# Kernel optimization log

Hardware: AMD Instinct MI355X
Metric: run time of the kernel (lower is better)

Reference implementation:

```python
import jax, jax.numpy as jnp
import numpy as np

B, N, IN_DIM, OUT_DIM = 16, 2048, 512, 512

def _xavier(key, shape):
    bound = float(np.sqrt(6.0 / (shape[0] + shape[1])))
    return jax.random.uniform(key, shape, jnp.float32, -bound, bound)

def setup_inputs() -> dict:
    key = jax.random.key(0)
    kx, kk, kq, kv = jax.random.split(key, 4)
    return {
        "x": jax.random.normal(kx, (B, N, IN_DIM), jnp.float32),
        "W_key": _xavier(kk, (IN_DIM, OUT_DIM)),
        "W_query": _xavier(kq, (IN_DIM, OUT_DIM)),
        "W_value": _xavier(kv, (IN_DIM, OUT_DIM)),
    }

def reference(x, W_key, W_query, W_value):
    # projections: [B, N, out_dim]
    k = jnp.matmul(x, W_key)
    q = jnp.matmul(x, W_query)
    v = jnp.matmul(x, W_value)
    scale = jnp.sqrt(jnp.asarray(IN_DIM, jnp.float32))
    scores = jnp.einsum("bnd,bmd->bnm", q, k) / scale  # [B, N, N]
    weights = jax.nn.softmax(scores, axis=2)
    attn = jnp.einsum("bnm,bmd->bnd", weights, v)  # [B, N, out_dim]
    return jnp.mean(attn, axis=1)  # [B, out_dim]
```

## Files before the change

### kernel.cpp

```cpp
#include <hip/hip_runtime.h>
#include <hip/hip_bf16.h>
#include <hip/hip_fp16.h>
#include <stdint.h>

#define NB 16
#define NN 2048
#define ND 512
#define SSCALE 0.044194173824159216f

typedef unsigned short u16;
typedef unsigned int u32;
typedef float f32x4 __attribute__((ext_vector_type(4)));
typedef __bf16 bf16x8 __attribute__((ext_vector_type(8)));
typedef unsigned short u16x8 __attribute__((ext_vector_type(8)));

__device__ __forceinline__ float bf2f(u16 h) {
  union { u32 u; float f; } v; v.u = ((u32)h) << 16; return v.f;
}
__device__ __forceinline__ u16 f2bf(float f) {
  union { float f; u32 u; } v; v.f = f;
  u32 r = v.u + 0x7fffu + ((v.u >> 16) & 1u);
  return (u16)(r >> 16);
}
__device__ __forceinline__ u16 f2h(float f) {
  __half h = __float2half(f);
  union { __half h; u16 u; } v; v.h = h; return v.u;
}
__device__ __forceinline__ float h2f(u16 u) {
  union { u16 u; __half h; } v; v.u = u; return __half2float(v.h);
}

__device__ __forceinline__ void async16(const void* g, void* l) {
  __builtin_amdgcn_global_load_lds(
      (const __attribute__((address_space(1))) u32*)g,
      (__attribute__((address_space(3))) u32*)l,
      16, 0, 0);
}

template <int MODE, bool AF32>
__global__ __launch_bounds__(256, 2) void gemm_bt(
    const void* __restrict__ Av, const u16* __restrict__ B, u16* __restrict__ C,
    float* __restrict__ Lrow, int lda, int ldb, int ldc, int K,
    long long sA, long long sB, long long sC, float cscale) {
  const int tid  = threadIdx.x;
  const int w    = tid >> 6;
  const int lane = tid & 63;
  const int wm   = w >> 1, wn = w & 1;
  const int lrow = lane & 15, quad = lane >> 4;
  const long long z = blockIdx.z;

  const float* Abf = (const float*)Av + z * sA + (size_t)blockIdx.y * 128 * lda;
  const u16*   Abh = (const u16*)Av   + z * sA + (size_t)blockIdx.y * 128 * lda;
  const u16*   Bb  = B + z * sB + (size_t)blockIdx.x * 128 * ldb;

  __shared__ __align__(16) u16 lds_a[128 * 32];
  __shared__ __align__(16) u16 lds_b[128 * 32];

  f32x4 acc[4][4];
#pragma unroll
  for (int i = 0; i < 4; i++)
#pragma unroll
    for (int j = 0; j < 4; j++) acc[i][j] = (f32x4){0.f, 0.f, 0.f, 0.f};

  for (int k0 = 0; k0 < K; k0 += 32) {
    if (k0) __syncthreads();
    if (AF32) {
      u16x8 va[2];
#pragma unroll
      for (int t = 0; t < 2; t++) {
        int ch  = t * 256 + tid;
        int row = ch >> 2;
        int cc  = (ch & 3) * 8;
        const float4* p = (const float4*)(Abf + (size_t)row * lda + k0 + cc);
        float4 f0 = p[0], f1 = p[1];
        u16x8 r;
        r[0] = f2bf(f0.x); r[1] = f2bf(f0.y); r[2] = f2bf(f0.z); r[3] = f2bf(f0.w);
        r[4] = f2bf(f1.x); r[5] = f2bf(f1.y); r[6] = f2bf(f1.z); r[7] = f2bf(f1.w);
        va[t] = r;
        async16(Bb + (size_t)row * ldb + k0 + cc, &lds_b[ch * 8]);
      }
#pragma unroll
      for (int t = 0; t < 2; t++) *(u16x8*)&lds_a[(t * 256 + tid) * 8] = va[t];
    } else {
#pragma unroll
      for (int t = 0; t < 2; t++) {
        int ch  = t * 256 + tid;
        int row = ch >> 2;
        int cc  = (ch & 3) * 8;
        async16(Abh + (size_t)row * lda + k0 + cc, &lds_a[ch * 8]);
        async16(Bb  + (size_t)row * ldb + k0 + cc, &lds_b[ch * 8]);
      }
    }
    __syncthreads();

    bf16x8 af[4], bfr[4];
#pragma unroll
    for (int i = 0; i < 4; i++) {
      af[i]  = *(const bf16x8*)&lds_a[(wm * 64 + i * 16 + lrow) * 32 + quad * 8];
      bfr[i] = *(const bf16x8*)&lds_b[(wn * 64 + i * 16 + lrow) * 32 + quad * 8];
    }
#pragma unroll
    for (int i = 0; i < 4; i++)
#pragma unroll
      for (int j = 0; j < 4; j++)
        acc[i][j] =
            __builtin_amdgcn_mfma_f32_16x16x32_bf16(af[i], bfr[j], acc[i][j], 0, 0, 0);
  }

  u16* Cb = C + z * sC + (size_t)blockIdx.y * 128 * ldc + (size_t)blockIdx.x * 128;
  if (MODE == 0) {
#pragma unroll
    for (int i = 0; i < 4; i++)
#pragma unroll
      for (int j = 0; j < 4; j++)
#pragma unroll
        for (int r = 0; r < 4; r++) {
          int row = wm * 64 + i * 16 + quad * 4 + r;
          int col = wn * 64 + j * 16 + lrow;
          Cb[(size_t)row * ldc + col] = f2bf(acc[i][j][r] * cscale);
        }
  } else {
    float* Lb = Lrow + z * NN + (size_t)blockIdx.y * 128;
#pragma unroll
    for (int i = 0; i < 4; i++)
#pragma unroll
      for (int r = 0; r < 4; r++) {
        int row = wm * 64 + i * 16 + quad * 4 + r;
        float rs = 0.f;
#pragma unroll
        for (int j = 0; j < 4; j++) {
          int col = wn * 64 + j * 16 + lrow;
          float e = __expf(fminf(acc[i][j][r] * cscale, 10.f));
          Cb[(size_t)row * ldc + col] = f2h(e);
          rs += e;
        }
        rs += __shfl_xor(rs, 1); rs += __shfl_xor(rs, 2);
        rs += __shfl_xor(rs, 4); rs += __shfl_xor(rs, 8);
        if (lrow == 0) atomicAdd(&Lb[row], rs);
      }
  }
}

__device__ __forceinline__ void stage_half(const u16* __restrict__ g, int ld,
                                           int row0, int k0,
                                           u16* __restrict__ l, int tid) {
  int r  = tid >> 3;
  int Lc = (tid & 7) ^ (r & 7);
  async16(g + (size_t)(row0 + r) * ld + k0 + Lc * 8, l + tid * 8);
  async16(g + (size_t)(row0 + 64 + r) * ld + k0 + Lc * 8, l + 4096 + tid * 8);
}

__device__ __forceinline__ bf16x8 ldf(const u16* __restrict__ h, int rbase,
                                      int lrow, int quad, int ks) {
  int rr = rbase + lrow;
  int pc = (ks * 4 + quad) ^ (lrow & 7);
  return *(const bf16x8*)&h[rr * 64 + pc * 8];
}

#define BAR() __builtin_amdgcn_s_barrier()
#define WAIT_LGKM()                                          \
  do {                                                       \
    asm volatile("s_waitcnt lgkmcnt(0)" ::: "memory");       \
    __builtin_amdgcn_sched_barrier(0);                       \
  } while (0)

#define READ_A(p, mh)                                                        \
  _Pragma("unroll") for (int i2 = 0; i2 < 4; ++i2)                           \
  _Pragma("unroll") for (int ks = 0; ks < 2; ++ks)                           \
      af[i2][ks] = ldf(sm + (p) * 32768 + wm * 8192, ((mh)*4 + i2) * 16,     \
                       lrow, quad, ks);

#define READ_B(p, nh)                                                        \
  _Pragma("unroll") for (int j2 = 0; j2 < 2; ++j2)                           \
  _Pragma("unroll") for (int ks = 0; ks < 2; ++ks)                           \
      bq[(nh)*2 + j2][ks] =                                                  \
          ldf(sm + (p) * 32768 + 16384 + (wn >> 1) * 8192,                   \
              (wn & 1) * 64 + ((nh)*2 + j2) * 16, lrow, quad, ks);

#define MFMA_Q(mh, nh)                                                       \
  __builtin_amdgcn_s_setprio(1);                                             \
  _Pragma("unroll") for (int i2 = 0; i2 < 4; ++i2)                           \
  _Pragma("unroll") for (int j2 = 0; j2 < 2; ++j2)                           \
  _Pragma("unroll") for (int ks = 0; ks < 2; ++ks)                           \
      acc[(mh)*4 + i2][(nh)*2 + j2] = __builtin_amdgcn_mfma_f32_16x16x32_bf16( \
          af[i2][ks], bq[(nh)*2 + j2][ks], acc[(mh)*4 + i2][(nh)*2 + j2],    \
          0, 0, 0);                                                          \
  __builtin_amdgcn_s_setprio(0);

#define STAGE_A(p, h, kt) \
  stage_half(Ab, lda, (h)*128, (kt)*64, sm + (p)*32768 + (h)*8192, tid)
#define STAGE_B(p, h, kt) \
  stage_half(Bb, ldb, (h)*128, (kt)*64, sm + (p)*32768 + 16384 + (h)*8192, tid)

template <int MODE>
__global__ __launch_bounds__(512, 2) void gemm256(
    const u16* __restrict__ A, const u16* __restrict__ B, u16* __restrict__ C,
    float* __restrict__ Lrow, int lda, int ldb, int ldc, int K,
    long long sA, long long sB, long long sC, float cscale) {
  const int tid  = threadIdx.x;
  const int wid  = tid >> 6, lane = tid & 63;
  const int wm   = wid >> 2, wn = wid & 3;
  const int lrow = lane & 15, quad = lane >> 4;

  const int bxx = blockIdx.x;
  const int byy = blockIdx.y;
  const long long z = blockIdx.z;

  const u16* Ab = A + z * sA + (size_t)byy * 256 * lda;
  const u16* Bb = B + z * sB + (size_t)bxx * 256 * ldb;

  __shared__ __align__(16) u16 sm[65536];

  f32x4 acc[8][4];
#pragma unroll
  for (int i = 0; i < 8; i++)
#pragma unroll
    for (int j = 0; j < 4; j++) acc[i][j] = (f32x4){0.f, 0.f, 0.f, 0.f};

  bf16x8 af[4][2];
  bf16x8 bq[4][2];

  const int NITER = K >> 7;

  STAGE_A(0, 0, 0); STAGE_A(0, 1, 0);
  STAGE_B(0, 0, 0); STAGE_B(0, 1, 0);
  STAGE_B(1, 0, 1); STAGE_B(1, 1, 1);
  asm volatile("s_waitcnt vmcnt(4)" ::: "memory");
  __builtin_amdgcn_sched_barrier(0);
  BAR();

  for (int it = 0; it < NITER; ++it) {
    const int t = 2 * it;
    const bool more = (it + 1 < NITER);

    READ_A(0, 0); READ_B(0, 0);
    STAGE_A(1, 0, t + 1);
    BAR(); WAIT_LGKM();
    MFMA_Q(0, 0);
    BAR();
    READ_B(0, 1);
    STAGE_A(1, 1, t + 1);
    BAR(); WAIT_LGKM();
    MFMA_Q(0, 1);
    BAR();
    READ_A(0, 1);
    if (more) STAGE_B(0, 0, t + 2);
    BAR(); WAIT_LGKM();
    MFMA_Q(1, 0);
    BAR();
    if (more) STAGE_B(0, 1, t + 2);
    BAR();
    MFMA_Q(1, 1);
    if (more) { asm volatile("s_waitcnt vmcnt(4)" ::: "memory"); }
    else      { asm volatile("s_waitcnt vmcnt(0)" ::: "memory"); }
    __builtin_amdgcn_sched_barrier(0);
    BAR();
    READ_A(1, 0); READ_B(1, 0);
    if (more) STAGE_A(0, 0, t + 2);
    BAR(); WAIT_LGKM();
    MFMA_Q(0, 0);
    BAR();
    READ_B(1, 1);
    if (more) STAGE_A(0, 1, t + 2);
    BAR(); WAIT_LGKM();
    MFMA_Q(0, 1);
    BAR();
    READ_A(1, 1);
    if (more) STAGE_B(1, 0, t + 3);
    BAR(); WAIT_LGKM();
    MFMA_Q(1, 0);
    BAR();
    if (more) STAGE_B(1, 1, t + 3);
    BAR();
    MFMA_Q(1, 1);
    if (more) {
      asm volatile("s_waitcnt vmcnt(4)" ::: "memory");
      __builtin_amdgcn_sched_barrier(0);
    }
    BAR();
  }

  u16* Cb = C + z * sC +
            (size_t)(byy * 256 + wm * 128) * ldc +
            (size_t)bxx * 256 + wn * 64;
  if (MODE == 0) {
#pragma unroll
    for (int i = 0; i < 8; i++)
#pragma unroll
      for (int j = 0; j < 4; j++)
#pragma unroll
        for (int r = 0; r < 4; r++) {
          int row = i * 16 + quad * 4 + r;
          int col = j * 16 + lrow;
          Cb[(size_t)row * ldc + col] = f2bf(acc[i][j][r] * cscale);
        }
  } else {
    float* Lb = Lrow + z * NN + (size_t)byy * 256 + wm * 128;
#pragma unroll
    for (int i = 0; i < 8; i++)
#pragma unroll
      for (int r = 0; r < 4; r++) {
        int row = i * 16 + quad * 4 + r;
        float rs = 0.f;
#pragma unroll
        for (int j = 0; j < 4; j++) {
          int col = j * 16 + lrow;
          float e = __expf(fminf(acc[i][j][r] * cscale, 10.f));
          Cb[(size_t)row * ldc + col] = f2h(e);
          rs += e;
        }
        rs += __shfl_xor(rs, 1); rs += __shfl_xor(rs, 2);
        rs += __shfl_xor(rs, 4); rs += __shfl_xor(rs, 8);
        if (lrow == 0) atomicAdd(&Lb[row], rs);
      }
  }
}

__global__ void cast_f32_bf16(const float* __restrict__ x, u16* __restrict__ xb) {
  size_t i = ((size_t)blockIdx.x * 256 + threadIdx.x) * 8;
  float4 f0 = *(const float4*)(x + i);
  float4 f1 = *(const float4*)(x + i + 4);
  u16x8 r;
  r[0] = f2bf(f0.x); r[1] = f2bf(f0.y); r[2] = f2bf(f0.z); r[3] = f2bf(f0.w);
  r[4] = f2bf(f1.x); r[5] = f2bf(f1.y); r[6] = f2bf(f1.z); r[7] = f2bf(f1.w);
  *(u16x8*)(xb + i) = r;
}

__global__ void col_sum(const __half* __restrict__ E, const float* __restrict__ L,
                        float* __restrict__ c) {
  int m8 = threadIdx.x * 8;
  int n0 = blockIdx.x * 128;
  int z  = blockIdx.y;
  const u16* Ep = (const u16*)E + ((size_t)z * NN + n0) * NN + m8;
  const float* lp = L + (size_t)z * NN + n0;
  float a[8] = {0.f, 0.f, 0.f, 0.f, 0.f, 0.f, 0.f, 0.f};
#pragma unroll 2
  for (int n = 0; n < 128; n++) {
    u16x8 h = *(const u16x8*)&Ep[(size_t)n * NN];
    float il = 1.0f / lp[n];
#pragma unroll
    for (int j = 0; j < 8; j++) a[j] += h2f(h[j]) * il;
  }
  float* cb = c + (size_t)z * NN + m8;
#pragma unroll
  for (int j = 0; j < 8; j++) atomicAdd(&cb[j], a[j]);
}

__global__ void tx_accum(const u16* __restrict__ xb, const float* __restrict__ c,
                         float* __restrict__ t) {
  int b = blockIdx.x, mc = blockIdx.y;
  int dgrp = threadIdx.x & 63;
  int mgrp = threadIdx.x >> 6;
  int d8 = dgrp * 8;
  const u16* vp = xb + ((size_t)b * NN + mc * 128 + mgrp * 32) * ND;
  const float* cp = c + b * NN + mc * 128 + mgrp * 32;
  float a[8] = {0.f, 0.f, 0.f, 0.f, 0.f, 0.f, 0.f, 0.f};
#pragma unroll 2
  for (int m = 0; m < 32; m++) {
    float cm = cp[m];
    u16x8 v = *(const u16x8*)&vp[(size_t)m * ND + d8];
#pragma unroll
    for (int j = 0; j < 8; j++) a[j] += cm * bf2f(v[j]);
  }
  __shared__ float smr[4][512];
#pragma unroll
  for (int j = 0; j < 8; j++) smr[mgrp][d8 + j] = a[j];
  __syncthreads();
  if (mgrp == 0) {
    float* tb = t + b * ND + d8;
#pragma unroll
    for (int j = 0; j < 8; j++)
      atomicAdd(&tb[j], a[j] + smr[1][d8 + j] + smr[2][d8 + j] + smr[3][d8 + j]);
  }
}

__global__ void final_wv(const float* __restrict__ t, const float* __restrict__ Wv,
                         float* __restrict__ out) {
  int b = blockIdx.x;
  int d = blockIdx.y * 64 + (threadIdx.x & 63);
  int lgrp = threadIdx.x >> 6;
  const float* tb = t + b * ND + lgrp * 128;
  const float* wp = Wv + (size_t)lgrp * 128 * ND + d;
  float a = 0.f;
#pragma unroll 4
  for (int l = 0; l < 128; l++) a += tb[l] * wp[(size_t)l * ND];
  __shared__ float smr[4][64];
  smr[lgrp][threadIdx.x & 63] = a;
  __syncthreads();
  if (lgrp == 0)
    out[b * ND + d] = (a + smr[1][threadIdx.x & 63] + smr[2][threadIdx.x & 63] +
                       smr[3][threadIdx.x & 63]) * (1.f / (float)NN);
}

extern "C" void kernel_launch(void* const* d_in, const int* in_sizes, int n_in,
                              void* d_out, int out_size, void* d_ws, size_t ws_size,
                              hipStream_t stream) {
  const float* x  = (const float*)d_in[0];
  const float* Wk = (const float*)d_in[1];
  const float* Wq = (const float*)d_in[2];
  const float* Wv = (const float*)d_in[3];
  float* out = (float*)d_out;

  char* ws = (char*)d_ws;
  size_t off = 0;
  float* L   = (float*)(ws + off); off += (size_t)NB * NN * 4;
  float* c   = (float*)(ws + off); off += (size_t)NB * NN * 4;
  float* t   = (float*)(ws + off); off += (size_t)NB * ND * 4;
  u16* Wqb   = (u16*)(ws + off);   off += (size_t)ND * ND * 2;
  u16* Mt    = (u16*)(ws + off);   off += (size_t)ND * ND * 2;
  const size_t small_total = off;

  const size_t XBSZ = (size_t)NB * NN * ND * 2;
  const size_t SB1  = (size_t)NN * NN * 2;
  u16* xb   = (u16*)(ws + small_total);
  u16* y    = (u16*)(ws + small_total + XBSZ);
  __half* E = (__half*)(ws + small_total + 2 * XBSZ);
  size_t srem = ws_size > small_total + 2 * XBSZ
              ? ws_size - small_total - 2 * XBSZ : 0;
  int chb = 0, sr = 128;
  if      (srem >= 16 * SB1) chb = 16;
  else if (srem >=  8 * SB1) chb = 8;
  else if (srem >=  4 * SB1) chb = 4;
  else if (srem >=  2 * SB1) chb = 2;
  else if (srem >=  1 * SB1) chb = 1;
  else {
    if      (srem >= (size_t)1024 * NN * 2) sr = 1024;
    else if (srem >= (size_t)512  * NN * 2) sr = 512;
    else if (srem >= (size_t)256  * NN * 2) sr = 256;
  }

  hipMemsetAsync(L, 0, (size_t)(2 * NB * NN + NB * ND) * sizeof(float), stream);

  cast_f32_bf16<<<8192, 256, 0, stream>>>(x, xb);
  cast_f32_bf16<<<128, 256, 0, stream>>>(Wq, Wqb);

  gemm_bt<0, true><<<dim3(4, 4, 1), 256, 0, stream>>>(
      Wk, Wqb, Mt, nullptr, ND, ND, ND, ND, 0, 0, 0, SSCALE);

  gemm256<0><<<dim3(2, 128, 1), 512, 0, stream>>>(
      xb, Mt, y, nullptr, ND, ND, ND, ND, 0, 0, 0, 1.0f);

  const long long sR = (long long)NN * ND;
  const long long sS = (long long)NN * NN;

  if (chb >= 1) {
    for (int cc = 0; cc < NB / chb; ++cc) {
      size_t o = (size_t)cc * chb * NN;
      gemm256<1><<<dim3(8, 8, chb), 512, 0, stream>>>(
          y + o * ND, xb + o * ND, (u16*)E, L + o, ND, ND, NN, ND,
          sR, sR, sS, 1.0f);
      col_sum<<<dim3(16, chb), 256, 0, stream>>>(E, L + o, c + o);
    }
  } else if (sr >= 256) {
    for (int b = 0; b < NB; ++b) {
      for (int ch = 0; ch < NN / sr; ++ch) {
        size_t o = (size_t)b * NN + (size_t)ch * sr;
        gemm256<1><<<dim3(8, sr / 256, 1), 512, 0, stream>>>(
            y + o * ND, xb + (size_t)b * NN * ND, (u16*)E, L + o,
            ND, ND, NN, ND, 0, 0, 0, 1.0f);
        col_sum<<<dim3(sr / 128, 1), 256, 0, stream>>>(E, L + o, c + b * NN);
      }
    }
  } else {
    for (int b = 0; b < NB; ++b) {
      for (int ch = 0; ch < NN / sr; ++ch) {
        size_t o = (size_t)b * NN + (size_t)ch * sr;
        gemm_bt<1, false><<<dim3(16, sr / 128, 1), 256, 0, stream>>>(
            y + o * ND, xb + (size_t)b * NN * ND, (u16*)E, L + o,
            ND, ND, NN, ND, 0, 0, 0, 1.0f);
        col_sum<<<dim3(sr / 128, 1), 256, 0, stream>>>(E, L + o, c + b * NN);
      }
    }
  }

  tx_accum<<<dim3(NB, 16), 256, 0, stream>>>(xb, c, t);
  final_wv<<<dim3(NB, 8), 256, 0, stream>>>(t, Wv, out);
  (void)in_sizes; (void)n_in; (void)out_size;
}
```

Measured before the change: 313.8 us.

## Make gemm256 persistent over multiple tiles with cross-tile prefetch

```diff
diff --git a/kernel.cpp b/kernel.cpp
--- a/kernel.cpp
+++ b/kernel.cpp
@@ -187,28 +187,22 @@
           0, 0, 0);                                                          \
   __builtin_amdgcn_s_setprio(0);
 
-#define STAGE_A(p, h, kt) \
-  stage_half(Ab, lda, (h)*128, (kt)*64, sm + (p)*32768 + (h)*8192, tid)
-#define STAGE_B(p, h, kt) \
-  stage_half(Bb, ldb, (h)*128, (kt)*64, sm + (p)*32768 + 16384 + (h)*8192, tid)
+#define STAGE_A(p, base, h, kt) \
+  stage_half(base, lda, (h)*128, (kt)*64, sm + (p)*32768 + (h)*8192, tid)
+#define STAGE_B(p, base, h, kt) \
+  stage_half(base, ldb, (h)*128, (kt)*64, sm + (p)*32768 + 16384 + (h)*8192, tid)
 
 template <int MODE>
 __global__ __launch_bounds__(512, 2) void gemm256(
     const u16* __restrict__ A, const u16* __restrict__ B, u16* __restrict__ C,
-    float* __restrict__ Lrow, int lda, int ldb, int ldc, int K,
+    float* __restrict__ Lrow, int lda, int ldb, int ldc,
+    int tpb, int tgxs, int tgys,
     long long sA, long long sB, long long sC, float cscale) {
   const int tid  = threadIdx.x;
   const int wid  = tid >> 6, lane = tid & 63;
   const int wm   = wid >> 2, wn = wid & 3;
   const int lrow = lane & 15, quad = lane >> 4;
 
-  const int bxx = blockIdx.x;
-  const int byy = blockIdx.y;
-  const long long z = blockIdx.z;
-
-  const u16* Ab = A + z * sA + (size_t)byy * 256 * lda;
-  const u16* Bb = B + z * sB + (size_t)bxx * 256 * ldb;
-
   __shared__ __align__(16) u16 sm[65536];
 
   f32x4 acc[8][4];
@@ -220,99 +214,137 @@
   bf16x8 af[4][2];
   bf16x8 bq[4][2];
 
-  const int NITER = K >> 7;
-
-  STAGE_A(0, 0, 0); STAGE_A(0, 1, 0);
-  STAGE_B(0, 0, 0); STAGE_B(0, 1, 0);
-  STAGE_B(1, 0, 1); STAGE_B(1, 1, 1);
+  const int t0    = blockIdx.x * tpb;
+  const int gmask = (1 << tgxs) - 1;
+  const int tmask = (1 << (tgxs + tgys)) - 1;
+
+  int bxxC, byyC; long long zC;
+  const u16 *AbC, *BbC;
+  {
+    zC = (long long)(t0 >> (tgxs + tgys));
+    int rem = t0 & tmask;
+    byyC = rem >> tgxs; bxxC = rem & gmask;
+    AbC = A + zC * sA + (size_t)byyC * 256 * lda;
+    BbC = B + zC * sB + (size_t)bxxC * 256 * ldb;
+  }
+
+  STAGE_A(0, AbC, 0, 0); STAGE_A(0, AbC, 1, 0);
+  STAGE_B(0, BbC, 0, 0); STAGE_B(0, BbC, 1, 0);
+  STAGE_B(1, BbC, 0, 1); STAGE_B(1, BbC, 1, 1);
   asm volatile("s_waitcnt vmcnt(4)" ::: "memory");
   __builtin_amdgcn_sched_barrier(0);
   BAR();
 
-  for (int it = 0; it < NITER; ++it) {
-    const int t = 2 * it;
-    const bool more = (it + 1 < NITER);
-
-    READ_A(0, 0); READ_B(0, 0);
-    STAGE_A(1, 0, t + 1);
-    BAR(); WAIT_LGKM();
-    MFMA_Q(0, 0);
-    BAR();
-    READ_B(0, 1);
-    STAGE_A(1, 1, t + 1);
-    BAR(); WAIT_LGKM();
-    MFMA_Q(0, 1);
-    BAR();
-    READ_A(0, 1);
-    if (more) STAGE_B(0, 0, t + 2);
-    BAR(); WAIT_LGKM();
-    MFMA_Q(1, 0);
-    BAR();
-    if (more) STAGE_B(0, 1, t + 2);
-    BAR();
-    MFMA_Q(1, 1);
-    if (more) { asm volatile("s_waitcnt vmcnt(4)" ::: "memory"); }
-    else      { asm volatile("s_waitcnt vmcnt(0)" ::: "memory"); }
-    __builtin_amdgcn_sched_barrier(0);
-    BAR();
-    READ_A(1, 0); READ_B(1, 0);
-    if (more) STAGE_A(0, 0, t + 2);
-    BAR(); WAIT_LGKM();
-    MFMA_Q(0, 0);
-    BAR();
-    READ_B(1, 1);
-    if (more) STAGE_A(0, 1, t + 2);
-    BAR(); WAIT_LGKM();
-    MFMA_Q(0, 1);
-    BAR();
-    READ_A(1, 1);
-    if (more) STAGE_B(1, 0, t + 3);
-    BAR(); WAIT_LGKM();
-    MFMA_Q(1, 0);
-    BAR();
-    if (more) STAGE_B(1, 1, t + 3);
-    BAR();
-    MFMA_Q(1, 1);
-    if (more) {
-      asm volatile("s_waitcnt vmcnt(4)" ::: "memory");
+  for (int ti = 0; ti < tpb; ++ti) {
+    const bool lastTile = (ti + 1 == tpb);
+    int bxxN = bxxC, byyN = byyC; long long zN = zC;
+    const u16 *AbN = AbC, *BbN = BbC;
+    if (!lastTile) {
+      int ot = t0 + ti + 1;
+      zN = (long long)(ot >> (tgxs + tgys));
+      int rem = ot & tmask;
+      byyN = rem >> tgxs; bxxN = rem & gmask;
+      AbN = A + zN * sA + (size_t)byyN * 256 * lda;
+      BbN = B + zN * sB + (size_t)bxxN * 256 * ldb;
+    }
+
+    for (int it = 0; it < 4; ++it) {
+      const int t = 2 * it;
+      const bool lastIt = (it == 3);
+      const bool more = !(lastIt && lastTile);
+      const u16* Ax = lastIt ? AbN : AbC;
+      const u16* Bx = lastIt ? BbN : BbC;
+      const int k2 = (t + 2) & 7, k3 = (t + 3) & 7;
+
+      READ_A(0, 0); READ_B(0, 0);
+      STAGE_A(1, AbC, 0, t + 1);
+      BAR(); WAIT_LGKM();
+      MFMA_Q(0, 0);
+      BAR();
+      READ_B(0, 1);
+      STAGE_A(1, AbC, 1, t + 1);
+      BAR(); WAIT_LGKM();
+      MFMA_Q(0, 1);
+      BAR();
+      READ_A(0, 1);
+      if (more) STAGE_B(0, Bx, 0, k2);
+      BAR(); WAIT_LGKM();
+      MFMA_Q(1, 0);
+      BAR();
+      if (more) STAGE_B(0, Bx, 1, k2);
+      BAR();
+      MFMA_Q(1, 1);
+      if (more) { asm volatile("s_waitcnt vmcnt(4)" ::: "memory"); }
+      else      { asm volatile("s_waitcnt vmcnt(0)" ::: "memory"); }
       __builtin_amdgcn_sched_barrier(0);
-    }
-    BAR();
-  }
-
-  u16* Cb = C + z * sC +
-            (size_t)(byy * 256 + wm * 128) * ldc +
-            (size_t)bxx * 256 + wn * 64;
-  if (MODE == 0) {
-#pragma unroll
-    for (int i = 0; i < 8; i++)
-#pragma unroll
-      for (int j = 0; j < 4; j++)
+      BAR();
+      READ_A(1, 0); READ_B(1, 0);
+      if (more) STAGE_A(0, Ax, 0, k2);
+      BAR(); WAIT_LGKM();
+      MFMA_Q(0, 0);
+      BAR();
+      READ_B(1, 1);
+      if (more) STAGE_A(0, Ax, 1, k2);
+      BAR(); WAIT_LGKM();
+      MFMA_Q(0, 1);
+      BAR();
+      READ_A(1, 1);
+      if (more) STAGE_B(1, Bx, 0, k3);
+      BAR(); WAIT_LGKM();
+      MFMA_Q(1, 0);
+      BAR();
+      if (more) STAGE_B(1, Bx, 1, k3);
+      BAR();
+      MFMA_Q(1, 1);
+      if (more) {
+        asm volatile("s_waitcnt vmcnt(4)" ::: "memory");
+        __builtin_amdgcn_sched_barrier(0);
+      }
+      BAR();
+    }
+
+    u16* Cb = C + zC * sC +
+              (size_t)(byyC * 256 + wm * 128) * ldc +
+              (size_t)bxxC * 256 + wn * 64;
+    if (MODE == 0) {
+#pragma unroll
+      for (int i = 0; i < 8; i++)
+#pragma unroll
+        for (int j = 0; j < 4; j++)
+#pragma unroll
+          for (int r = 0; r < 4; r++) {
+            int row = i * 16 + quad * 4 + r;
+            int col = j * 16 + lrow;
+            Cb[(size_t)row * ldc + col] = f2bf(acc[i][j][r] * cscale);
+          }
+    } else {
+      float* Lb = Lrow + zC * NN + (size_t)byyC * 256 + wm * 128;
+#pragma unroll
+      for (int i = 0; i < 8; i++)
 #pragma unroll
         for (int r = 0; r < 4; r++) {
           int row = i * 16 + quad * 4 + r;
-          int col = j * 16 + lrow;
-          Cb[(size_t)row * ldc + col] = f2bf(acc[i][j][r] * cscale);
+          float rs = 0.f;
+#pragma unroll
+          for (int j = 0; j < 4; j++) {
+            int col = j * 16 + lrow;
+            float e = __expf(fminf(acc[i][j][r] * cscale, 10.f));
+            Cb[(size_t)row * ldc + col] = f2h(e);
+            rs += e;
+          }
+          rs += __shfl_xor(rs, 1); rs += __shfl_xor(rs, 2);
+          rs += __shfl_xor(rs, 4); rs += __shfl_xor(rs, 8);
+          if (lrow == 0) atomicAdd(&Lb[row], rs);
         }
-  } else {
-    float* Lb = Lrow + z * NN + (size_t)byy * 256 + wm * 128;
-#pragma unroll
-    for (int i = 0; i < 8; i++)
-#pragma unroll
-      for (int r = 0; r < 4; r++) {
-        int row = i * 16 + quad * 4 + r;
-        float rs = 0.f;
-#pragma unroll
-        for (int j = 0; j < 4; j++) {
-          int col = j * 16 + lrow;
-          float e = __expf(fminf(acc[i][j][r] * cscale, 10.f));
-          Cb[(size_t)row * ldc + col] = f2h(e);
-          rs += e;
-        }
-        rs += __shfl_xor(rs, 1); rs += __shfl_xor(rs, 2);
-        rs += __shfl_xor(rs, 4); rs += __shfl_xor(rs, 8);
-        if (lrow == 0) atomicAdd(&Lb[row], rs);
-      }
+    }
+
+    if (!lastTile) {
+#pragma unroll
+      for (int i = 0; i < 8; i++)
+#pragma unroll
+        for (int j = 0; j < 4; j++) acc[i][j] = (f32x4){0.f, 0.f, 0.f, 0.f};
+    }
+    bxxC = bxxN; byyC = byyN; zC = zN; AbC = AbN; BbC = BbN;
   }
 }
 
@@ -437,8 +469,8 @@
   gemm_bt<0, true><<<dim3(4, 4, 1), 256, 0, stream>>>(
       Wk, Wqb, Mt, nullptr, ND, ND, ND, ND, 0, 0, 0, SSCALE);
 
-  gemm256<0><<<dim3(2, 128, 1), 512, 0, stream>>>(
-      xb, Mt, y, nullptr, ND, ND, ND, ND, 0, 0, 0, 1.0f);
+  gemm256<0><<<dim3(256, 1, 1), 512, 0, stream>>>(
+      xb, Mt, y, nullptr, ND, ND, ND, 1, 1, 7, 0, 0, 0, 1.0f);
 
   const long long sR = (long long)NN * ND;
   const long long sS = (long long)NN * NN;
@@ -446,18 +478,21 @@
   if (chb >= 1) {
     for (int cc = 0; cc < NB / chb; ++cc) {
       size_t o = (size_t)cc * chb * NN;
-      gemm256<1><<<dim3(8, 8, chb), 512, 0, stream>>>(
-          y + o * ND, xb + o * ND, (u16*)E, L + o, ND, ND, NN, ND,
-          sR, sR, sS, 1.0f);
+      int tiles = 64 * chb;
+      int tpb   = tiles >= 1024 ? 4 : (tiles >= 512 ? 2 : 1);
+      gemm256<1><<<dim3(tiles / tpb, 1, 1), 512, 0, stream>>>(
+          y + o * ND, xb + o * ND, (u16*)E, L + o, ND, ND, NN,
+          tpb, 3, 3, sR, sR, sS, 1.0f);
       col_sum<<<dim3(16, chb), 256, 0, stream>>>(E, L + o, c + o);
     }
   } else if (sr >= 256) {
     for (int b = 0; b < NB; ++b) {
       for (int ch = 0; ch < NN / sr; ++ch) {
         size_t o = (size_t)b * NN + (size_t)ch * sr;
-        gemm256<1><<<dim3(8, sr / 256, 1), 512, 0, stream>>>(
+        int tgys = (sr == 1024) ? 2 : (sr == 512) ? 1 : 0;
+        gemm256<1><<<dim3(8 << tgys, 1, 1), 512, 0, stream>>>(
             y + o * ND, xb + (size_t)b * NN * ND, (u16*)E, L + o,
-            ND, ND, NN, ND, 0, 0, 0, 1.0f);
+            ND, ND, NN, 1, 3, tgys, 0, 0, 0, 1.0f);
         col_sum<<<dim3(sr / 128, 1), 256, 0, stream>>>(E, L + o, c + b * NN);
       }
     }
```

New measurement: 405.1 us. 1.29x slower.
